# Optimization experiments

Hardware: AMD Instinct MI355X
Metric: run time of the kernel (lower is better)

The kernel has to match this reference:

```python
import jax, jax.numpy as jnp
import numpy as np

B, T, C = 4, 4096, 1024
H, G = 16, 8
HS = C // H      # head size = 64
GT = T // G      # group_t = 512
KAPX = 1         # k_apx


def causal_attn(q, k, v):
    # q,k,v: [..., L, d]; causal softmax attention within last two dims
    d = q.shape[-1]
    s = jnp.einsum('...qd,...kd->...qk', q, k) / jnp.sqrt(jnp.asarray(d, q.dtype))
    mask = jnp.tril(jnp.ones((s.shape[-2], s.shape[-1]), dtype=bool))
    s = jnp.where(mask, s, jnp.asarray(-1e30, s.dtype))
    return jnp.einsum('...qk,...kd->...qd', jax.nn.softmax(s, axis=-1), v)


def apply_rope(x, cos, sin):
    # x: [B,H,T,HS]; cos/sin: [T,HS//2]; interleaved (even,odd) complex pairs
    xr = x.reshape(x.shape[:-1] + (HS // 2, 2))
    r, i = xr[..., 0], xr[..., 1]
    c = cos[None, None]
    s = sin[None, None]
    return jnp.stack([r * c - i * s, r * s + i * c], axis=-1).reshape(x.shape)


def setup_inputs() -> dict:
    key = jax.random.key(0)
    k1, k2, k3, k4, k5, k6 = jax.random.split(key, 6)
    x = jax.random.normal(k1, (B, T, C), jnp.float32)
    lim = 1.0 / np.sqrt(C)
    Wqkv = jax.random.uniform(k2, (C, 3 * C), jnp.float32, -lim, lim)
    Wo = jax.random.uniform(k3, (C, C), jnp.float32, -lim, lim)
    # init_() uses std = 1/sqrt(last_dim) = 1/sqrt(k_apx) = 1
    q_proj = jax.random.uniform(k4, (GT, KAPX), jnp.float32, -1.0, 1.0)
    k_proj = jax.random.uniform(k5, (GT, KAPX), jnp.float32, -1.0, 1.0)
    v_proj = jax.random.uniform(k6, (GT, KAPX), jnp.float32, -1.0, 1.0)
    inv = 1.0 / (10000.0 ** (np.arange(0, HS, 2) / HS))
    ang = np.outer(np.arange(T), inv)
    freqs_cos = jnp.asarray(np.cos(ang), jnp.float32)
    freqs_sin = jnp.asarray(np.sin(ang), jnp.float32)
    return dict(x=x, Wqkv=Wqkv, Wo=Wo, q_proj=q_proj, k_proj=k_proj,
                v_proj=v_proj, freqs_cos=freqs_cos, freqs_sin=freqs_sin)


def reference(x, Wqkv, Wo, q_proj, k_proj, v_proj, freqs_cos, freqs_sin):
    q, k, v = jnp.split(x @ Wqkv, 3, axis=-1)          # each [B,T,C]
    q = q.reshape(B, T, H, HS).transpose(0, 2, 1, 3)    # [B,H,T,HS]
    k = k.reshape(B, T, H, HS).transpose(0, 2, 1, 3)
    q = apply_rope(q, freqs_cos, freqs_sin)
    k = apply_rope(k, freqs_cos, freqs_sin)
    # torch .view on contiguous [B,H,T,HS]: raw row-major reinterpretation
    q = q.reshape(B, G, GT, H, HS).transpose(0, 3, 1, 2, 4)  # [B,H,G,GT,HS]
    k = k.reshape(B, G, GT, H, HS).transpose(0, 3, 1, 2, 4)
    v = v.reshape(B, G, GT, H, HS).transpose(0, 3, 1, 2, 4)  # v viewed from [B,T,C]
    # its_time branch: learned time-pooling of all but last group
    qb = jnp.einsum('bhgtc,tk->bhgkc', q[:, :, :-1], q_proj)  # [B,H,G-1,1,HS]
    kb = jnp.einsum('bhgtc,tk->bhgkc', k[:, :, :-1], k_proj)
    vb = jnp.einsum('bhgtc,tk->bhgkc', v[:, :, :-1], v_proj)
    o = causal_attn(q, k, v)          # block-local causal attention [B,H,G,GT,HS]
    vb = causal_attn(qb, kb, vb)      # compressed block attention [B,H,G-1,1,HS]
    o = o.reshape(B, H, G * GT, HS).transpose(0, 2, 1, 3).reshape(B, T, C)
    out = o @ Wo                       # dropout=0 (eval)
    return (out, qb, kb, vb)
```

## Files before the change

kernel.cpp:

```cpp
#include <hip/hip_runtime.h>


typedef float  float4_t  __attribute__((ext_vector_type(4)));
typedef short  bfrag     __attribute__((ext_vector_type(8)));
typedef unsigned short ushort8 __attribute__((ext_vector_type(8)));

#define MFMA_BF16(A, B, C) __builtin_amdgcn_mfma_f32_16x16x32_bf16((A), (B), (C), 0, 0, 0)

__device__ __forceinline__ unsigned short f2bf(float f) {
  union { float f; unsigned u; } v; v.f = f;
  return (unsigned short)((v.u + 0x7FFFu + ((v.u >> 16) & 1u)) >> 16);
}
__device__ __forceinline__ float bf2f(unsigned short h) {
  union { unsigned u; float f; } v; v.u = ((unsigned)h) << 16; return v.f;
}
__device__ __forceinline__ void async16(const void* g, void* l) {
  __builtin_amdgcn_global_load_lds(
      (const __attribute__((address_space(1))) unsigned int*)(unsigned long long)g,
      (__attribute__((address_space(3))) unsigned int*)(unsigned long long)l,
      16, 0, 0);
}

__global__ __launch_bounds__(256) void cvt_kernel(const float* __restrict__ in,
                                                  unsigned short* __restrict__ out, int n8) {
  int i = blockIdx.x * 256 + threadIdx.x;
  if (i >= n8) return;
  const float4_t* p = (const float4_t*)in + (size_t)i * 2;
  float4_t a = p[0], c = p[1];
  ushort8 r;
  r[0] = f2bf(a[0]); r[1] = f2bf(a[1]); r[2] = f2bf(a[2]); r[3] = f2bf(a[3]);
  r[4] = f2bf(c[0]); r[5] = f2bf(c[1]); r[6] = f2bf(c[2]); r[7] = f2bf(c[3]);
  *((ushort8*)out + i) = r;
}

__global__ void transpose_cvt_kernel(const float* __restrict__ in,
                                     unsigned short* __restrict__ out, int R, int C) {
  __shared__ float t[32][33];
  int bc = blockIdx.x * 32, br = blockIdx.y * 32;
  int x = threadIdx.x, y = threadIdx.y;
  for (int i = 0; i < 32; i += 8) t[y + i][x] = in[(size_t)(br + y + i) * C + bc + x];
  __syncthreads();
  for (int i = 0; i < 32; i += 8) out[(size_t)(bc + y + i) * R + br + x] = f2bf(t[x][y + i]);
}

__global__ void transpose2_f32_kernel(const float* __restrict__ a,
                                      const float* __restrict__ b,
                                      float* __restrict__ oa, float* __restrict__ ob_,
                                      int R, int C) {
  const float* in = blockIdx.z ? b : a;
  float* out = blockIdx.z ? ob_ : oa;
  __shared__ float t[32][33];
  int bc = blockIdx.x * 32, br = blockIdx.y * 32;
  int x = threadIdx.x, y = threadIdx.y;
  for (int i = 0; i < 32; i += 8) t[y + i][x] = in[(size_t)(br + y + i) * C + bc + x];
  __syncthreads();
  for (int i = 0; i < 32; i += 8) out[(size_t)(bc + y + i) * R + br + x] = t[x][y + i];
}

__device__ __forceinline__ void gemm_core(const unsigned short* __restrict__ A,
                                          const unsigned short* __restrict__ BT,
                                          int bm0, int bn0, int K,
                                          unsigned short* As, unsigned short* Bs,
                                          float4_t acc[2][4]) {
  int tid = threadIdx.x, w = tid >> 6;
  int lane = tid & 63, quad = lane >> 4, l16 = lane & 15;
  int wm = w >> 1, wn = w & 1;
  int r = tid >> 3, x = tid & 7;
  int sc = (x ^ (r & 7)) * 8;
  for (int k0 = 0; k0 < K; k0 += 64) {
    __syncthreads();
#pragma unroll
    for (int c = 0; c < 2; ++c) {
      async16(&A [(size_t)(bm0 + c * 64 + r) * K + k0 + sc], &As[(size_t)(c * 512 + tid) * 8]);
      async16(&BT[(size_t)(bn0 + c * 64 + r) * K + k0 + sc], &Bs[(size_t)(c * 512 + tid) * 8]);
    }
    __syncthreads();
#pragma unroll
    for (int ks = 0; ks < 2; ++ks) {
      bfrag af[2], bf_[4];
#pragma unroll
      for (int i = 0; i < 2; ++i) {
        int rm = wm * 32 + i * 16 + l16;
        af[i]  = *(const bfrag*)&As[(size_t)(rm * 8 + ((ks * 4 + quad) ^ (rm & 7))) * 8];
      }
#pragma unroll
      for (int j = 0; j < 4; ++j) {
        int rn = wn * 64 + j * 16 + l16;
        bf_[j] = *(const bfrag*)&Bs[(size_t)(rn * 8 + ((ks * 4 + quad) ^ (rn & 7))) * 8];
      }
#pragma unroll
      for (int i = 0; i < 2; ++i)
#pragma unroll
        for (int j = 0; j < 4; ++j)
          acc[i][j] = MFMA_BF16(af[i], bf_[j], acc[i][j]);
    }
  }
}

__global__ __launch_bounds__(512, 4) void gemm1_kernel(const unsigned short* __restrict__ xb,
    const unsigned short* __restrict__ wqkvT,
    const float* __restrict__ fcT, const float* __restrict__ fsT,
    unsigned short* __restrict__ qkv) {
  __shared__ __align__(16) unsigned char smem[34816];
  unsigned short* As = (unsigned short*)smem;
  unsigned short* Bs = (unsigned short*)(smem + 16384);
  float4_t acc[2][4];
  for (int i = 0; i < 2; ++i) for (int j = 0; j < 4; ++j)
    acc[i][j] = (float4_t){0.f, 0.f, 0.f, 0.f};
  int lin = blockIdx.y * 24 + blockIdx.x;
  int swz = (lin & 7) * 384 + (lin >> 3);
  int bn0 = (swz % 24) * 128, bm0 = (swz / 24) * 128;
  gemm_core(xb, wqkvT, bm0, bn0, 1024, As, Bs, acc);

  int tid = threadIdx.x, w = tid >> 6, lane = tid & 63, quad = lane >> 4, l16 = lane & 15;
  int wm = w >> 1, wn = w & 1;

  for (int i = 0; i < 2; ++i) {
    int t0 = (bm0 + wm * 32 + i * 16 + quad * 4) & 4095;
    for (int j = 0; j < 4; ++j) {
      int gcol = bn0 + wn * 64 + j * 16 + l16;
      if (gcol < 2048) {
        int ci = (gcol & 63) >> 1;
        const float4_t c4 = *(const float4_t*)&fcT[(size_t)ci * 4096 + t0];
        const float4_t s4 = *(const float4_t*)&fsT[(size_t)ci * 4096 + t0];
        for (int r = 0; r < 4; ++r) {
          float val = acc[i][j][r];
          float partner = __shfl_xor(val, 1);
          float c = c4[r], s = s4[r];
          acc[i][j][r] = (gcol & 1) ? fmaf(partner, s, val * c)
                                    : fmaf(-partner, s, val * c);
        }
      }
    }
  }

  __syncthreads();
  float* Es = (float*)smem;
  float* slice = &Es[w * 1088];
  for (int i = 0; i < 2; ++i) {
    for (int j = 0; j < 4; ++j)
      for (int r = 0; r < 4; ++r)
        slice[(quad * 4 + r) * 68 + j * 16 + l16] = acc[i][j][r];
    for (int m = 0; m < 2; ++m) {
      int rl = m * 8 + (lane >> 3);
      int cb = (lane & 7) * 8;
      const float* rp = &slice[rl * 68 + cb];
      ushort8 outv;
      outv[0] = f2bf(rp[0]); outv[1] = f2bf(rp[1]);
      outv[2] = f2bf(rp[2]); outv[3] = f2bf(rp[3]);
      outv[4] = f2bf(rp[4]); outv[5] = f2bf(rp[5]);
      outv[6] = f2bf(rp[6]); outv[7] = f2bf(rp[7]);
      int grow = bm0 + wm * 32 + i * 16 + rl;
      int gcol = bn0 + wn * 64 + cb;
      *(ushort8*)&qkv[(size_t)grow * 3072 + gcol] = outv;
    }
  }
}

__global__ __launch_bounds__(512, 4) void gemm2_kernel(const unsigned short* __restrict__ ob,
    const unsigned short* __restrict__ woT, float* __restrict__ outp) {
  __shared__ __align__(16) unsigned short As[128 * 64];
  __shared__ __align__(16) unsigned short Bs[128 * 64];
  float4_t acc[2][4];
  for (int i = 0; i < 2; ++i) for (int j = 0; j < 4; ++j)
    acc[i][j] = (float4_t){0.f, 0.f, 0.f, 0.f};
  int lin = blockIdx.y * 8 + blockIdx.x;
  int swz = (lin & 7) * 128 + (lin >> 3);
  int bn0 = (swz & 7) * 128, bm0 = (swz >> 3) * 128;
  gemm_core(ob, woT, bm0, bn0, 1024, As, Bs, acc);
  int tid = threadIdx.x, w = tid >> 6, lane = tid & 63, quad = lane >> 4, l16 = lane & 15;
  int wm = w >> 1, wn = w & 1;
  for (int i = 0; i < 2; ++i)
    for (int j = 0; j < 4; ++j)
      for (int r = 0; r < 4; ++r)
        outp[(size_t)(bm0 + wm * 32 + i * 16 + quad * 4 + r) * 1024 +
             bn0 + wn * 64 + j * 16 + l16] = acc[i][j][r];
}

__global__ __launch_bounds__(512) void attn_kernel(const unsigned short* __restrict__ qkv,
    unsigned short* __restrict__ ob) {
  __shared__ __align__(16) unsigned short Ks[128 * 64];
  __shared__ __align__(16) unsigned short VTs[64 * 136];
  __shared__ __align__(16) unsigned short Ps[8 * 16 * 136];
  int lin = blockIdx.x;
  int bx = (lin & 7) * 256 + (lin >> 3);
  int qt2 = bx & 3, g = (bx >> 2) & 7, h = (bx >> 5) & 15, b = bx >> 9;
  int tid = threadIdx.x, w = tid >> 6, lane = tid & 63, quad = lane >> 4, l16 = lane & 15;

  const unsigned short* QKb = qkv + ((size_t)b * 4096 + h) * 3072 + g * 128;
  const unsigned short* Vb  = qkv + ((size_t)(b * 4096 + g * 512)) * 3072 + 2048 + h * 64;

  int qrow = qt2 * 128 + w * 16 + l16;
  const unsigned short* Qr = QKb + ((size_t)((qrow & 255) << 4)) * 3072 + (qrow >> 8) * 64;
  bfrag qf0 = *(const bfrag*)&Qr[quad * 8];
  bfrag qf1 = *(const bfrag*)&Qr[32 + quad * 8];

  float4_t acc[4];
#pragma unroll
  for (int i = 0; i < 4; ++i) acc[i] = (float4_t){0.f, 0.f, 0.f, 0.f};
  float m_i[4] = {-1e30f, -1e30f, -1e30f, -1e30f};
  float l_i[4] = {0.f, 0.f, 0.f, 0.f};

  int skey = tid >> 3, sx = tid & 7, ss = sx ^ (skey & 7);
  int kp = tid & 63, hsg = tid >> 6;
  unsigned short* Pw = &Ps[w * 2176];
  int ntiles = qt2 + 1;

  ushort8 kreg0, kreg1, vreg0, vreg1;

  {
    int krow0 = skey, krow1 = 64 + skey;
    kreg0 = *(const ushort8*)&QKb[((size_t)((krow0 & 255) << 4)) * 3072 + (krow0 >> 8) * 64 + 1024 + ss * 8];
    kreg1 = *(const ushort8*)&QKb[((size_t)((krow1 & 255) << 4)) * 3072 + (krow1 >> 8) * 64 + 1024 + ss * 8];
    const unsigned short* vp0 = Vb + (size_t)(kp * 2) * 3072 + hsg * 8;
    vreg0 = *(const ushort8*)vp0;
    vreg1 = *(const ushort8*)(vp0 + 3072);
    *(ushort8*)&Ks[(size_t)(tid) * 8]       = kreg0;
    *(ushort8*)&Ks[(size_t)(512 + tid) * 8] = kreg1;
#pragma unroll
    for (int e = 0; e < 8; ++e)
      *(unsigned*)&VTs[(size_t)(hsg * 8 + e) * 136 + kp * 2] =
          (unsigned)vreg0[e] | ((unsigned)vreg1[e] << 16);
  }

  for (int kt = 0; kt < ntiles; ++kt) {
    __syncthreads();

    float4_t s[8];
#pragma unroll
    for (int c = 0; c < 8; ++c) s[c] = (float4_t){0.f, 0.f, 0.f, 0.f};
    {
      int sl0 = l16 * 8 + (quad ^ (l16 & 7));
      int sl1 = l16 * 8 + ((4 + quad) ^ (l16 & 7));
#pragma unroll
      for (int c = 0; c < 8; ++c) {
        s[c] = MFMA_BF16(qf0, *(const bfrag*)&Ks[(size_t)(sl0 + 128 * c) * 8], s[c]);
        s[c] = MFMA_BF16(qf1, *(const bfrag*)&Ks[(size_t)(sl1 + 128 * c) * 8], s[c]);
      }
    }

    bool more = (kt + 1 < ntiles);
    if (more) {
      int kb = (kt + 1) * 128;
      int krow0 = kb + skey, krow1 = kb + 64 + skey;
      kreg0 = *(const ushort8*)&QKb[((size_t)((krow0 & 255) << 4)) * 3072 + (krow0 >> 8) * 64 + 1024 + ss * 8];
      kreg1 = *(const ushort8*)&QKb[((size_t)((krow1 & 255) << 4)) * 3072 + (krow1 >> 8) * 64 + 1024 + ss * 8];
      const unsigned short* vp0 = Vb + (size_t)(kb + kp * 2) * 3072 + hsg * 8;
      vreg0 = *(const ushort8*)vp0;
      vreg1 = *(const ushort8*)(vp0 + 3072);
    }

    int qa = qt2 * 128 + w * 16 + quad * 4;
    int kb0 = kt * 128 + l16;
#pragma unroll
    for (int r = 0; r < 4; ++r) {
      float vv[8];
#pragma unroll
      for (int c = 0; c < 8; ++c) {
        vv[c] = s[c][r] * 0.125f;
        if (kb0 + 16 * c > qa + r) vv[c] = -1e30f;
      }
      float tm = fmaxf(fmaxf(fmaxf(vv[0], vv[1]), fmaxf(vv[2], vv[3])),
                       fmaxf(fmaxf(vv[4], vv[5]), fmaxf(vv[6], vv[7])));
      tm = fmaxf(tm, __shfl_xor(tm, 1));
      tm = fmaxf(tm, __shfl_xor(tm, 2));
      tm = fmaxf(tm, __shfl_xor(tm, 4));
      tm = fmaxf(tm, __shfl_xor(tm, 8));
      float nm = fmaxf(m_i[r], tm);
      float alpha = __expf(m_i[r] - nm);
      m_i[r] = nm;
      float p[8], rs = 0.f;
#pragma unroll
      for (int c = 0; c < 8; ++c) { p[c] = __expf(vv[c] - nm); rs += p[c]; }
      rs += __shfl_xor(rs, 1);
      rs += __shfl_xor(rs, 2);
      rs += __shfl_xor(rs, 4);
      rs += __shfl_xor(rs, 8);
      l_i[r] = l_i[r] * alpha + rs;
      acc[0][r] *= alpha; acc[1][r] *= alpha; acc[2][r] *= alpha; acc[3][r] *= alpha;
      int pr = (quad * 4 + r) * 136 + l16;
#pragma unroll
      for (int c = 0; c < 8; ++c) Pw[pr + 16 * c] = f2bf(p[c]);
    }
    bfrag pf[4];
#pragma unroll
    for (int c = 0; c < 4; ++c)
      pf[c] = *(const bfrag*)&Pw[(size_t)l16 * 136 + 32 * c + quad * 8];
#pragma unroll
    for (int ht = 0; ht < 4; ++ht) {
#pragma unroll
      for (int c = 0; c < 4; ++c) {
        bfrag vf = *(const bfrag*)&VTs[(size_t)(ht * 16 + l16) * 136 + 32 * c + quad * 8];
        acc[ht] = MFMA_BF16(pf[c], vf, acc[ht]);
      }
    }

    __syncthreads();
    if (more) {
      *(ushort8*)&Ks[(size_t)(tid) * 8]       = kreg0;
      *(ushort8*)&Ks[(size_t)(512 + tid) * 8] = kreg1;
#pragma unroll
      for (int e = 0; e < 8; ++e)
        *(unsigned*)&VTs[(size_t)(hsg * 8 + e) * 136 + kp * 2] =
            (unsigned)vreg0[e] | ((unsigned)vreg1[e] << 16);
    }
  }

  int orow = b * 4096 + g * 512 + qt2 * 128 + w * 16 + quad * 4;
#pragma unroll
  for (int ht = 0; ht < 4; ++ht)
#pragma unroll
    for (int r = 0; r < 4; ++r)
      ob[(size_t)(orow + r) * 1024 + h * 64 + ht * 16 + l16] = f2bf(acc[ht][r] / l_i[r]);
}

__global__ __launch_bounds__(1024) void pools_kernel(const unsigned short* __restrict__ qkv,
    const float* __restrict__ qp, const float* __restrict__ kp,
    const float* __restrict__ vp, float* __restrict__ outp) {
  __shared__ float red[3][16][64];
  int g = blockIdx.x, h = blockIdx.y, b = blockIdx.z;
  int hs = threadIdx.x & 63, tc = threadIdx.x >> 6;
  const unsigned short* qb_ = qkv + ((size_t)b * 4096 + h) * 3072 + g * 128 + hs;
  const unsigned short* vb_ = qkv + ((size_t)(b * 4096 + g * 512)) * 3072 + 2048 + h * 64 + hs;
  float aq = 0.f, ak = 0.f, av = 0.f;
  int t0 = tc * 32;
  for (int t = t0; t < t0 + 32; ++t) {
    size_t qoff = ((size_t)((t & 255) << 4)) * 3072 + (t >> 8) * 64;
    aq = fmaf(bf2f(qb_[qoff]), qp[t], aq);
    ak = fmaf(bf2f(qb_[qoff + 1024]), kp[t], ak);
    av = fmaf(bf2f(vb_[(size_t)t * 3072]), vp[t], av);
  }
  red[0][tc][hs] = aq;
  red[1][tc][hs] = ak;
  red[2][tc][hs] = av;
  __syncthreads();
  if (tc < 3) {
    float a = 0.f;
    for (int c = 0; c < 16; ++c) a += red[tc][c][hs];
    size_t oi = (((size_t)b * 16 + h) * 7 + g) * 64 + hs;
    size_t off = (tc == 0) ? 0 : (tc == 1) ? 28672 : 57344;
    outp[16777216 + off + oi] = a;
  }
}

extern "C" void kernel_launch(void* const* d_in, const int* in_sizes, int n_in,
                              void* d_out, int out_size, void* d_ws, size_t ws_size,
                              hipStream_t stream) {
  (void)in_sizes; (void)n_in; (void)out_size; (void)ws_size;
  const float* x    = (const float*)d_in[0];
  const float* Wqkv = (const float*)d_in[1];
  const float* Wo   = (const float*)d_in[2];
  const float* qp   = (const float*)d_in[3];
  const float* kp   = (const float*)d_in[4];
  const float* vp   = (const float*)d_in[5];
  const float* fc   = (const float*)d_in[6];
  const float* fs   = (const float*)d_in[7];
  float* outp = (float*)d_out;

  char* ws = (char*)d_ws;
  unsigned short* xb    = (unsigned short*)(ws);
  unsigned short* wqkvT = (unsigned short*)(ws + 33554432);
  unsigned short* woT   = (unsigned short*)(ws + 39845888);
  unsigned short* qkv   = (unsigned short*)(ws + 41943040);
  unsigned short* ob    = xb;

  float* fcT = outp;
  float* fsT = outp + 131072;

  cvt_kernel<<<8192, 256, 0, stream>>>(x, xb, 2097152);
  transpose_cvt_kernel<<<dim3(96, 32), dim3(32, 8), 0, stream>>>(Wqkv, wqkvT, 1024, 3072);
  transpose_cvt_kernel<<<dim3(32, 32), dim3(32, 8), 0, stream>>>(Wo, woT, 1024, 1024);
  transpose2_f32_kernel<<<dim3(1, 128, 2), dim3(32, 8), 0, stream>>>(fc, fs, fcT, fsT, 4096, 32);
  gemm1_kernel<<<dim3(24, 128), 512, 0, stream>>>(xb, wqkvT, fcT, fsT, qkv);
  attn_kernel<<<2048, 512, 0, stream>>>(qkv, ob);
  pools_kernel<<<dim3(7, 16, 4), 1024, 0, stream>>>(qkv, qp, kp, vp, outp);
  gemm2_kernel<<<dim3(8, 128), 512, 0, stream>>>(ob, woT, outp);
}
```

Baseline: 411.3 us.

## Merge prep kernels, fold pooling into attention launch, remap GEMM tile order

The four preprocessing kernels (x conversion, the two weight transposes and the rope table transpose) become one launch that dispatches on block index. The pooling kernel becomes extra 512-thread blocks appended to the attention grid, each running 64 timesteps per thread. Both GEMMs also get a new block-to-tile mapping that groups consecutive blocks over 16 M tiles sharing an N column, changing L2 reuse. This removes several launch gaps and lets the small pooling work overlap attention, but adds a branch in the prep kernel and uneven block sizes in the attention grid.

```diff
diff --git a/kernel.cpp b/kernel.cpp
--- a/kernel.cpp
+++ b/kernel.cpp
@@ -21,40 +21,37 @@
       16, 0, 0);
 }
 
-__global__ __launch_bounds__(256) void cvt_kernel(const float* __restrict__ in,
-                                                  unsigned short* __restrict__ out, int n8) {
-  int i = blockIdx.x * 256 + threadIdx.x;
-  if (i >= n8) return;
-  const float4_t* p = (const float4_t*)in + (size_t)i * 2;
-  float4_t a = p[0], c = p[1];
-  ushort8 r;
-  r[0] = f2bf(a[0]); r[1] = f2bf(a[1]); r[2] = f2bf(a[2]); r[3] = f2bf(a[3]);
-  r[4] = f2bf(c[0]); r[5] = f2bf(c[1]); r[6] = f2bf(c[2]); r[7] = f2bf(c[3]);
-  *((ushort8*)out + i) = r;
-}
-
-__global__ void transpose_cvt_kernel(const float* __restrict__ in,
-                                     unsigned short* __restrict__ out, int R, int C) {
+__global__ __launch_bounds__(256) void prep_kernel(
+    const float* __restrict__ x, unsigned short* __restrict__ xb,
+    const float* __restrict__ Wqkv, unsigned short* __restrict__ wqkvT,
+    const float* __restrict__ Wo, unsigned short* __restrict__ woT,
+    const float* __restrict__ fc, const float* __restrict__ fs,
+    float* __restrict__ fcT, float* __restrict__ fsT) {
+  int idx = blockIdx.x;
+  int tx = threadIdx.x, ty = threadIdx.y;
+  int tid = ty * 32 + tx;
+  if (idx < 8192) {
+    int i = idx * 256 + tid;
+    const float4_t* p = (const float4_t*)x + (size_t)i * 2;
+    float4_t a = p[0], c = p[1];
+    ushort8 r;
+    r[0] = f2bf(a[0]); r[1] = f2bf(a[1]); r[2] = f2bf(a[2]); r[3] = f2bf(a[3]);
+    r[4] = f2bf(c[0]); r[5] = f2bf(c[1]); r[6] = f2bf(c[2]); r[7] = f2bf(c[3]);
+    *((ushort8*)xb + i) = r;
+    return;
+  }
   __shared__ float t[32][33];
-  int bc = blockIdx.x * 32, br = blockIdx.y * 32;
-  int x = threadIdx.x, y = threadIdx.y;
-  for (int i = 0; i < 32; i += 8) t[y + i][x] = in[(size_t)(br + y + i) * C + bc + x];
+  const float* in; float* outf = nullptr; unsigned short* outh = nullptr;
+  int R, C, bx, by;
+  if (idx < 11264)      { int k = idx - 8192;  in = Wqkv; outh = wqkvT; R = 1024; C = 3072; bx = k % 96; by = k / 96; }
+  else if (idx < 12288) { int k = idx - 11264; in = Wo;   outh = woT;   R = 1024; C = 1024; bx = k % 32; by = k / 32; }
+  else                  { int k = idx - 12288; in = (k >= 128) ? fs : fc; outf = (k >= 128) ? fsT : fcT;
+                          R = 4096; C = 32; bx = 0; by = k & 127; }
+  int bc = bx * 32, br = by * 32;
+  for (int i = 0; i < 32; i += 8) t[ty + i][tx] = in[(size_t)(br + ty + i) * C + bc + tx];
   __syncthreads();
-  for (int i = 0; i < 32; i += 8) out[(size_t)(bc + y + i) * R + br + x] = f2bf(t[x][y + i]);
-}
-
-__global__ void transpose2_f32_kernel(const float* __restrict__ a,
-                                      const float* __restrict__ b,
-                                      float* __restrict__ oa, float* __restrict__ ob_,
-                                      int R, int C) {
-  const float* in = blockIdx.z ? b : a;
-  float* out = blockIdx.z ? ob_ : oa;
-  __shared__ float t[32][33];
-  int bc = blockIdx.x * 32, br = blockIdx.y * 32;
-  int x = threadIdx.x, y = threadIdx.y;
-  for (int i = 0; i < 32; i += 8) t[y + i][x] = in[(size_t)(br + y + i) * C + bc + x];
-  __syncthreads();
-  for (int i = 0; i < 32; i += 8) out[(size_t)(bc + y + i) * R + br + x] = t[x][y + i];
+  if (outh) { for (int i = 0; i < 32; i += 8) outh[(size_t)(bc + ty + i) * R + br + tx] = f2bf(t[tx][ty + i]); }
+  else      { for (int i = 0; i < 32; i += 8) outf[(size_t)(bc + ty + i) * R + br + tx] = t[tx][ty + i]; }
 }
 
 __device__ __forceinline__ void gemm_core(const unsigned short* __restrict__ A,
@@ -108,8 +105,9 @@
   for (int i = 0; i < 2; ++i) for (int j = 0; j < 4; ++j)
     acc[i][j] = (float4_t){0.f, 0.f, 0.f, 0.f};
   int lin = blockIdx.y * 24 + blockIdx.x;
-  int swz = (lin & 7) * 384 + (lin >> 3);
-  int bn0 = (swz % 24) * 128, bm0 = (swz / 24) * 128;
+  int q = lin & 7, rem = lin >> 3;
+  int bn0 = (rem / 16) * 128;
+  int bm0 = (q * 16 + (rem & 15)) * 128;
   gemm_core(xb, wqkvT, bm0, bn0, 1024, As, Bs, acc);
 
   int tid = threadIdx.x, w = tid >> 6, lane = tid & 63, quad = lane >> 4, l16 = lane & 15;
@@ -165,8 +163,9 @@
   for (int i = 0; i < 2; ++i) for (int j = 0; j < 4; ++j)
     acc[i][j] = (float4_t){0.f, 0.f, 0.f, 0.f};
   int lin = blockIdx.y * 8 + blockIdx.x;
-  int swz = (lin & 7) * 128 + (lin >> 3);
-  int bn0 = (swz & 7) * 128, bm0 = (swz >> 3) * 128;
+  int q = lin & 7, rem = lin >> 3;
+  int bn0 = (rem / 16) * 128;
+  int bm0 = (q * 16 + (rem & 15)) * 128;
   gemm_core(ob, woT, bm0, bn0, 1024, As, Bs, acc);
   int tid = threadIdx.x, w = tid >> 6, lane = tid & 63, quad = lane >> 4, l16 = lane & 15;
   int wm = w >> 1, wn = w & 1;
@@ -178,14 +177,46 @@
 }
 
 __global__ __launch_bounds__(512) void attn_kernel(const unsigned short* __restrict__ qkv,
-    unsigned short* __restrict__ ob) {
+    unsigned short* __restrict__ ob,
+    const float* __restrict__ qp, const float* __restrict__ kp,
+    const float* __restrict__ vp, float* __restrict__ outp) {
   __shared__ __align__(16) unsigned short Ks[128 * 64];
   __shared__ __align__(16) unsigned short VTs[64 * 136];
   __shared__ __align__(16) unsigned short Ps[8 * 16 * 136];
   int lin = blockIdx.x;
+  int tid = threadIdx.x;
+
+  if (lin >= 2048) {
+    float* red = (float*)Ks;
+    int pid = lin - 2048;
+    int g = pid % 7, h = (pid / 7) % 16, b = pid / 112;
+    int hs = tid & 63, tc = tid >> 6;
+    const unsigned short* qb_ = qkv + ((size_t)b * 4096 + h) * 3072 + g * 128 + hs;
+    const unsigned short* vb_ = qkv + ((size_t)(b * 4096 + g * 512)) * 3072 + 2048 + h * 64 + hs;
+    float aq = 0.f, ak = 0.f, av = 0.f;
+    for (int t = tc * 64; t < tc * 64 + 64; ++t) {
+      size_t qoff = ((size_t)((t & 255) << 4)) * 3072 + (t >> 8) * 64;
+      aq = fmaf(bf2f(qb_[qoff]), qp[t], aq);
+      ak = fmaf(bf2f(qb_[qoff + 1024]), kp[t], ak);
+      av = fmaf(bf2f(vb_[(size_t)t * 3072]), vp[t], av);
+    }
+    red[(0 * 8 + tc) * 64 + hs] = aq;
+    red[(1 * 8 + tc) * 64 + hs] = ak;
+    red[(2 * 8 + tc) * 64 + hs] = av;
+    __syncthreads();
+    if (tc < 3) {
+      float a = 0.f;
+      for (int c = 0; c < 8; ++c) a += red[(tc * 8 + c) * 64 + hs];
+      size_t oi = (((size_t)b * 16 + h) * 7 + g) * 64 + hs;
+      size_t off = (tc == 0) ? 0 : (tc == 1) ? 28672 : 57344;
+      outp[16777216 + off + oi] = a;
+    }
+    return;
+  }
+
   int bx = (lin & 7) * 256 + (lin >> 3);
   int qt2 = bx & 3, g = (bx >> 2) & 7, h = (bx >> 5) & 15, b = bx >> 9;
-  int tid = threadIdx.x, w = tid >> 6, lane = tid & 63, quad = lane >> 4, l16 = lane & 15;
+  int w = tid >> 6, lane = tid & 63, quad = lane >> 4, l16 = lane & 15;
 
   const unsigned short* QKb = qkv + ((size_t)b * 4096 + h) * 3072 + g * 128;
   const unsigned short* Vb  = qkv + ((size_t)(b * 4096 + g * 512)) * 3072 + 2048 + h * 64;
@@ -202,7 +233,7 @@
   float l_i[4] = {0.f, 0.f, 0.f, 0.f};
 
   int skey = tid >> 3, sx = tid & 7, ss = sx ^ (skey & 7);
-  int kp = tid & 63, hsg = tid >> 6;
+  int kp2 = tid & 63, hsg = tid >> 6;
   unsigned short* Pw = &Ps[w * 2176];
   int ntiles = qt2 + 1;
 
@@ -212,14 +243,14 @@
     int krow0 = skey, krow1 = 64 + skey;
     kreg0 = *(const ushort8*)&QKb[((size_t)((krow0 & 255) << 4)) * 3072 + (krow0 >> 8) * 64 + 1024 + ss * 8];
     kreg1 = *(const ushort8*)&QKb[((size_t)((krow1 & 255) << 4)) * 3072 + (krow1 >> 8) * 64 + 1024 + ss * 8];
-    const unsigned short* vp0 = Vb + (size_t)(kp * 2) * 3072 + hsg * 8;
+    const unsigned short* vp0 = Vb + (size_t)(kp2 * 2) * 3072 + hsg * 8;
     vreg0 = *(const ushort8*)vp0;
     vreg1 = *(const ushort8*)(vp0 + 3072);
     *(ushort8*)&Ks[(size_t)(tid) * 8]       = kreg0;
     *(ushort8*)&Ks[(size_t)(512 + tid) * 8] = kreg1;
 #pragma unroll
     for (int e = 0; e < 8; ++e)
-      *(unsigned*)&VTs[(size_t)(hsg * 8 + e) * 136 + kp * 2] =
+      *(unsigned*)&VTs[(size_t)(hsg * 8 + e) * 136 + kp2 * 2] =
           (unsigned)vreg0[e] | ((unsigned)vreg1[e] << 16);
   }
 
@@ -245,7 +276,7 @@
       int krow0 = kb + skey, krow1 = kb + 64 + skey;
       kreg0 = *(const ushort8*)&QKb[((size_t)((krow0 & 255) << 4)) * 3072 + (krow0 >> 8) * 64 + 1024 + ss * 8];
       kreg1 = *(const ushort8*)&QKb[((size_t)((krow1 & 255) << 4)) * 3072 + (krow1 >> 8) * 64 + 1024 + ss * 8];
-      const unsigned short* vp0 = Vb + (size_t)(kb + kp * 2) * 3072 + hsg * 8;
+      const unsigned short* vp0 = Vb + (size_t)(kb + kp2 * 2) * 3072 + hsg * 8;
       vreg0 = *(const ushort8*)vp0;
       vreg1 = *(const ushort8*)(vp0 + 3072);
     }
@@ -301,7 +332,7 @@
       *(ushort8*)&Ks[(size_t)(512 + tid) * 8] = kreg1;
 #pragma unroll
       for (int e = 0; e < 8; ++e)
-        *(unsigned*)&VTs[(size_t)(hsg * 8 + e) * 136 + kp * 2] =
+        *(unsigned*)&VTs[(size_t)(hsg * 8 + e) * 136 + kp2 * 2] =
             (unsigned)vreg0[e] | ((unsigned)vreg1[e] << 16);
     }
   }
@@ -312,35 +343,6 @@
 #pragma unroll
     for (int r = 0; r < 4; ++r)
       ob[(size_t)(orow + r) * 1024 + h * 64 + ht * 16 + l16] = f2bf(acc[ht][r] / l_i[r]);
-}
-
-__global__ __launch_bounds__(1024) void pools_kernel(const unsigned short* __restrict__ qkv,
-    const float* __restrict__ qp, const float* __restrict__ kp,
-    const float* __restrict__ vp, float* __restrict__ outp) {
-  __shared__ float red[3][16][64];
-  int g = blockIdx.x, h = blockIdx.y, b = blockIdx.z;
-  int hs = threadIdx.x & 63, tc = threadIdx.x >> 6;
-  const unsigned short* qb_ = qkv + ((size_t)b * 4096 + h) * 3072 + g * 128 + hs;
-  const unsigned short* vb_ = qkv + ((size_t)(b * 4096 + g * 512)) * 3072 + 2048 + h * 64 + hs;
-  float aq = 0.f, ak = 0.f, av = 0.f;
-  int t0 = tc * 32;
-  for (int t = t0; t < t0 + 32; ++t) {
-    size_t qoff = ((size_t)((t & 255) << 4)) * 3072 + (t >> 8) * 64;
-    aq = fmaf(bf2f(qb_[qoff]), qp[t], aq);
-    ak = fmaf(bf2f(qb_[qoff + 1024]), kp[t], ak);
-    av = fmaf(bf2f(vb_[(size_t)t * 3072]), vp[t], av);
-  }
-  red[0][tc][hs] = aq;
-  red[1][tc][hs] = ak;
-  red[2][tc][hs] = av;
-  __syncthreads();
-  if (tc < 3) {
-    float a = 0.f;
-    for (int c = 0; c < 16; ++c) a += red[tc][c][hs];
-    size_t oi = (((size_t)b * 16 + h) * 7 + g) * 64 + hs;
-    size_t off = (tc == 0) ? 0 : (tc == 1) ? 28672 : 57344;
-    outp[16777216 + off + oi] = a;
-  }
 }
 
 extern "C" void kernel_launch(void* const* d_in, const int* in_sizes, int n_in,
@@ -367,12 +369,9 @@
   float* fcT = outp;
   float* fsT = outp + 131072;
 
-  cvt_kernel<<<8192, 256, 0, stream>>>(x, xb, 2097152);
-  transpose_cvt_kernel<<<dim3(96, 32), dim3(32, 8), 0, stream>>>(Wqkv, wqkvT, 1024, 3072);
-  transpose_cvt_kernel<<<dim3(32, 32), dim3(32, 8), 0, stream>>>(Wo, woT, 1024, 1024);
-  transpose2_f32_kernel<<<dim3(1, 128, 2), dim3(32, 8), 0, stream>>>(fc, fs, fcT, fsT, 4096, 32);
+  prep_kernel<<<12544, dim3(32, 8), 0, stream>>>(x, xb, Wqkv, wqkvT, Wo, woT,
+                                                 fc, fs, fcT, fsT);
   gemm1_kernel<<<dim3(24, 128), 512, 0, stream>>>(xb, wqkvT, fcT, fsT, qkv);
-  attn_kernel<<<2048, 512, 0, stream>>>(qkv, ob);
-  pools_kernel<<<dim3(7, 16, 4), 1024, 0, stream>>>(qkv, qp, kp, vp, outp);
+  attn_kernel<<<2496, 512, 0, stream>>>(qkv, ob, qp, kp, vp, outp);
   gemm2_kernel<<<dim3(8, 128), 512, 0, stream>>>(ob, woT, outp);
 }
```

After: 450.4 us. +9.5%, slower.
